# Kernel optimization log

Measured on AMD Instinct MI355X. Metric: run time of the kernel, lower is better.

## Reference

```python
import jax, jax.numpy as jnp
import numpy as np

D_MODEL = 1024
NUM_HEADS = 16
D_K = D_MODEL // NUM_HEADS


def setup_inputs() -> dict:
    key = jax.random.key(0)
    ks = jax.random.split(key, 9)
    s = 1.0 / np.sqrt(D_MODEL)
    x = jax.random.normal(ks[0], (2, 2048, D_MODEL), dtype=jnp.float32)
    Wq = jax.random.uniform(ks[1], (D_MODEL, D_MODEL), jnp.float32, -s, s)
    bq = jax.random.uniform(ks[2], (D_MODEL,), jnp.float32, -s, s)
    Wk = jax.random.uniform(ks[3], (D_MODEL, D_MODEL), jnp.float32, -s, s)
    bk = jax.random.uniform(ks[4], (D_MODEL,), jnp.float32, -s, s)
    Wv = jax.random.uniform(ks[5], (D_MODEL, D_MODEL), jnp.float32, -s, s)
    bv = jax.random.uniform(ks[6], (D_MODEL,), jnp.float32, -s, s)
    Wo = jax.random.uniform(ks[7], (D_MODEL, D_MODEL), jnp.float32, -s, s)
    bo = jax.random.uniform(ks[8], (D_MODEL,), jnp.float32, -s, s)
    return {"x": x, "Wq": Wq, "bq": bq, "Wk": Wk, "bk": bk,
            "Wv": Wv, "bv": bv, "Wo": Wo, "bo": bo}


def reference(x, Wq, bq, Wk, bk, Wv, bv, Wo, bo):
    B, S, _ = x.shape
    # projections (torch Linear: x @ W.T + b; here W stored as [in, out])
    q = (x @ Wq + bq).reshape(B, S, NUM_HEADS, D_K).transpose(0, 2, 1, 3)
    k = (x @ Wk + bk).reshape(B, S, NUM_HEADS, D_K).transpose(0, 2, 1, 3)
    v = (x @ Wv + bv).reshape(B, S, NUM_HEADS, D_K).transpose(0, 2, 1, 3)
    scores = jnp.einsum('bhqd,bhkd->bhqk', q, k) / jnp.sqrt(jnp.float32(D_K))
    attn = jax.nn.softmax(scores, axis=-1)
    out = jnp.einsum('bhqk,bhkd->bhqd', attn, v)  # [B,H,S,Dk]
    out = out.transpose(0, 2, 1, 3).reshape(B, S, D_MODEL)
    return out @ Wo + bo
```

## Files before the change

kernel.cpp:

```cpp
#include <hip/hip_runtime.h>
#include <hip/hip_bf16.h>

#define SEQ   2048
#define DM    1024
#define NH    16
#define DK    64
#define BATCH 2
#define M_TOT 4096
#define C1 0.18033688011112042f

typedef __attribute__((ext_vector_type(8))) short bf16x8;
typedef __attribute__((ext_vector_type(4))) float f32x4;
typedef __attribute__((ext_vector_type(16))) float f32x16;
typedef __attribute__((ext_vector_type(2))) int i32x2;
typedef unsigned short u16;

__device__ inline u16 f2b(float f) {
    union { float f; unsigned u; } x; x.f = f;
    return (u16)((x.u + 0x7FFFu + ((x.u >> 16) & 1u)) >> 16);
}

__device__ inline unsigned pk2(float a, float b) {
    __hip_bfloat162 h = __float22bfloat162_rn(make_float2(a, b));
    return *reinterpret_cast<unsigned*>(&h);
}

__device__ inline void async_cp16(const u16* g, u16* l) {
    __builtin_amdgcn_global_load_lds(
        (const __attribute__((address_space(1))) unsigned int*)g,
        (__attribute__((address_space(3))) unsigned int*)l, 16, 0, 0);
}

__device__ inline f32x16 zero16() {
    f32x16 z;
    #pragma unroll
    for (int i = 0; i < 16; ++i) z[i] = 0.f;
    return z;
}

__device__ inline bf16x8 mk8(unsigned a, unsigned b, unsigned c, unsigned d) {
    union { unsigned u[4]; bf16x8 v; } x;
    x.u[0] = a; x.u[1] = b; x.u[2] = c; x.u[3] = d;
    return x.v;
}

#define MFMA32(a, b, c) __builtin_amdgcn_mfma_f32_32x32x16_bf16(a, b, c, 0, 0, 0)

__global__ __launch_bounds__(256) void cast_x(
    const float4* __restrict__ x, uint2* __restrict__ xb)
{
    int gid = blockIdx.x * 256 + threadIdx.x;
    float4 v = x[gid];
    uint2 o;
    o.x = pk2(v.x, v.y); o.y = pk2(v.z, v.w);
    xb[gid] = o;
}

__global__ __launch_bounds__(256) void transpose_cast4(
    const float* __restrict__ W0, const float* __restrict__ W1,
    const float* __restrict__ W2, const float* __restrict__ W3,
    u16* __restrict__ WtBase)
{
    __shared__ float tile[32][33];
    const int t = threadIdx.x;
    const int n0 = blockIdx.x << 5, k0 = blockIdx.y << 5, z = blockIdx.z;
    const float* W = (z == 0) ? W0 : (z == 1) ? W1 : (z == 2) ? W2 : W3;
    u16* Wt = WtBase + (size_t)z * DM * DM;
    #pragma unroll
    for (int i = 0; i < 4; ++i) {
        int idx = t + (i << 8); int r = idx >> 5, c = idx & 31;
        tile[r][c] = W[(size_t)(k0 + r) * DM + n0 + c];
    }
    __syncthreads();
    #pragma unroll
    for (int i = 0; i < 4; ++i) {
        int idx = t + (i << 8); int r = idx >> 5, c = idx & 31;
        Wt[(size_t)(n0 + r) * DM + k0 + c] = f2b(tile[c][r]);
    }
}

__global__ __launch_bounds__(256) void gemm_bt(
    const u16* __restrict__ A, const u16* __restrict__ Bt, int mode,
    const float* __restrict__ bias0, const float* __restrict__ bias1,
    const float* __restrict__ bias2,
    void* __restrict__ out0, void* __restrict__ out1, void* __restrict__ out2)
{
    __shared__ u16 sh[16896];
    u16* As = sh;
    u16* Bs = sh + 8192;
    const int t = threadIdx.x, wid = t >> 6, lane = t & 63;
    const int lr = lane & 15, quad = lane >> 4;
    const int m0 = blockIdx.y << 7, n0 = blockIdx.x << 7;
    const int wm = (wid & 1) << 6, wn = (wid >> 1) << 6;
    const int rowA = lane >> 2;
    const int colA = (((lane & 3) - ((lane >> 3) & 3)) & 3) << 3;
    const int sA = (((lr >> 1) + quad) & 3) << 3;

    f32x4 acc[4][4];
    #pragma unroll
    for (int i = 0; i < 4; ++i)
        #pragma unroll
        for (int j = 0; j < 4; ++j) acc[i][j] = (f32x4){0.f, 0.f, 0.f, 0.f};

    auto stage = [&](int k0s, int buf) {
        #pragma unroll
        for (int i = 0; i < 2; ++i) {
            int ch = wid * 2 + i;
            async_cp16(A  + (size_t)(m0 + ch * 16 + rowA) * DM + k0s + colA,
                       As + buf * 4096 + ch * 16 * 32);
            async_cp16(Bt + (size_t)(n0 + ch * 16 + rowA) * DM + k0s + colA,
                       Bs + buf * 4096 + ch * 16 * 32);
        }
    };

    stage(0, 0);
    __syncthreads();

    for (int k0 = 0; k0 < DM; k0 += 32) {
        const int cur = (k0 >> 5) & 1;
        if (k0 + 32 < DM) stage(k0 + 32, cur ^ 1);

        const u16* Ac = As + cur * 4096;
        const u16* Bc = Bs + cur * 4096;
        bf16x8 af[4], bfr[4];
        #pragma unroll
        for (int mt = 0; mt < 4; ++mt)
            af[mt] = *(const bf16x8*)(Ac + (wm + 16 * mt + lr) * 32 + sA);
        #pragma unroll
        for (int nt = 0; nt < 4; ++nt)
            bfr[nt] = *(const bf16x8*)(Bc + (wn + 16 * nt + lr) * 32 + sA);
        #pragma unroll
        for (int mt = 0; mt < 4; ++mt)
            #pragma unroll
            for (int nt = 0; nt < 4; ++nt)
                acc[mt][nt] = __builtin_amdgcn_mfma_f32_16x16x32_bf16(
                    af[mt], bfr[nt], acc[mt][nt], 0, 0, 0);
        __syncthreads();
    }

    if (mode == 1) {
        u16* wstrip = sh + wid * 1152;
        const int ngb = n0 + wn;
        const int which = ngb >> 10, nnb = ngb & 1023;
        const int h = nnb >> 6;
        const float* bp = (which == 0) ? bias0 : (which == 1) ? bias1 : bias2;
        const float sc = (which == 0) ? C1 : 1.0f;
        float bias_v[4];
        #pragma unroll
        for (int nt = 0; nt < 4; ++nt) bias_v[nt] = bp[nnb + 16 * nt + lr];

        if (which != 1) {
            u16* dst = (which == 0) ? (u16*)out0 : (u16*)out2;
            #pragma unroll
            for (int mt = 0; mt < 4; ++mt) {
                #pragma unroll
                for (int nt = 0; nt < 4; ++nt) {
                    uint2 w;
                    w.x = pk2((acc[mt][nt][0] + bias_v[nt]) * sc,
                              (acc[mt][nt][1] + bias_v[nt]) * sc);
                    w.y = pk2((acc[mt][nt][2] + bias_v[nt]) * sc,
                              (acc[mt][nt][3] + bias_v[nt]) * sc);
                    *(uint2*)(wstrip + (16 * nt + lr) * 16 + quad * 4) = w;
                }
                asm volatile("s_waitcnt lgkmcnt(0)" ::: "memory");
                #pragma unroll
                for (int half = 0; half < 2; ++half) {
                    int id = lane + 64 * half;
                    int d = id >> 1, cho = (id & 1) << 3;
                    int m = m0 + wm + 16 * mt + cho;
                    int b = m >> 11, s = m & (SEQ - 1);
                    *(uint4*)(dst + ((size_t)(b * NH + h) * DK + d) * SEQ + s) =
                        *(const uint4*)(wstrip + d * 16 + cho);
                }
                asm volatile("s_waitcnt lgkmcnt(0)" ::: "memory");
            }
        } else {
            u16* dst = (u16*)out1;
            #pragma unroll
            for (int mt = 0; mt < 4; ++mt) {
                #pragma unroll
                for (int nt = 0; nt < 4; ++nt)
                    #pragma unroll
                    for (int r = 0; r < 4; ++r)
                        wstrip[(quad * 4 + r) * 72 + 16 * nt + lr] =
                            f2b(acc[mt][nt][r] + bias_v[nt]);
                asm volatile("s_waitcnt lgkmcnt(0)" ::: "memory");
                #pragma unroll
                for (int half = 0; half < 2; ++half) {
                    int id = lane + 64 * half;
                    int mloc = id >> 3, dl = (id & 7) << 3;
                    int m = m0 + wm + 16 * mt + mloc;
                    int b = m >> 11, s = m & (SEQ - 1);
                    *(uint4*)(dst + ((size_t)(b * NH + h) * SEQ + s) * DK + dl) =
                        *(const uint4*)(wstrip + mloc * 72 + dl);
                }
                asm volatile("s_waitcnt lgkmcnt(0)" ::: "memory");
            }
        }
    } else {
        float* O = (float*)out0;
        float* strip = (float*)sh + wid * 1088;
        float bias_v[4];
        #pragma unroll
        for (int nt = 0; nt < 4; ++nt) bias_v[nt] = bias0[n0 + wn + 16 * nt + lr];
        #pragma unroll
        for (int mt = 0; mt < 4; ++mt) {
            #pragma unroll
            for (int nt = 0; nt < 4; ++nt)
                #pragma unroll
                for (int r = 0; r < 4; ++r)
                    strip[(quad * 4 + r) * 68 + 16 * nt + lr] =
                        acc[mt][nt][r] + bias_v[nt];
            asm volatile("s_waitcnt lgkmcnt(0)" ::: "memory");
            #pragma unroll
            for (int rr = 0; rr < 4; ++rr) {
                int row = lane >> 2, chunk = (lane & 3) + 4 * rr;
                float4 v = *(const float4*)(strip + row * 68 + chunk * 4);
                *(float4*)(O + (size_t)(m0 + wm + 16 * mt + row) * DM
                             + n0 + wn + chunk * 4) = v;
            }
            asm volatile("s_waitcnt lgkmcnt(0)" ::: "memory");
        }
    }
}

__global__ __launch_bounds__(512) void attn_mfma(
    const u16* __restrict__ Qt, const u16* __restrict__ K,
    const u16* __restrict__ Vt, u16* __restrict__ A)
{
    __shared__ u16 sh[33280];

    const int t = threadIdx.x, wid = t >> 6, lane = t & 63;
    const int l31 = lane & 31, hi = lane >> 5, l7 = lane & 7;
    const int g = wid >> 2, wq = wid & 3;
    const int bx = blockIdx.x;
    const int xcd = bx & 7, within = bx >> 3;
    const int bh  = xcd * 4 + (within >> 4);
    const int q0  = (within & 15) << 7;

    const u16* Kb = K  + (size_t)bh * SEQ * DK;
    const u16* Vb = Vt + (size_t)bh * DK * SEQ;

    const int qw = q0 + 32 * wq + l31;
    const u16* Qb = Qt + (size_t)bh * DK * SEQ + qw;
    bf16x8 bQ[4];
    #pragma unroll
    for (int s = 0; s < 4; ++s)
        #pragma unroll
        for (int j = 0; j < 8; ++j)
            bQ[s][j] = (short)Qb[(size_t)(16 * s + 8 * hi + j) * SEQ];

    f32x16 O0 = zero16(), O1 = zero16();
    float lr = 0.f;

    const int w8row = wid * 8 + (lane >> 3);
    const int scol  = ((l7 ^ (lane >> 3)) << 3);

    const int rA = l31 * 64;
    int cks[4];
    #pragma unroll
    for (int s = 0; s < 4; ++s) cks[s] = ((2 * s + hi) ^ l7) << 3;

    auto stage = [&](int sit, int buf) {
        const int kt = sit << 7;
        u16* kd = sh + (buf << 13) + wid * 512;
        u16* vd = sh + 16384 + (buf << 13) + wid * 512;
        async_cp16(Kb + (size_t)(kt + w8row) * DK + scol,       kd);
        async_cp16(Kb + (size_t)(kt + 64 + w8row) * DK + scol,  kd + 4096);
        async_cp16(Vb + (size_t)w8row * SEQ + kt + scol,        vd);
        async_cp16(Vb + (size_t)w8row * SEQ + kt + 64 + scol,   vd + 4096);
    };

    stage(0, 0);
    __syncthreads();

    for (int sit = 0; sit < SEQ / 128; ++sit) {
        const u16* kbp = sh + ((sit & 1) << 13) + (g << 12) + rA;
        const u16* vbp = sh + 16384 + ((sit & 1) << 13) + (g << 12) + rA;
        if (sit + 1 < SEQ / 128) stage(sit + 1, (sit + 1) & 1);

        f32x16 Sv[2];
        __builtin_amdgcn_s_setprio(1);
        {
            bf16x8 a;
            Sv[0] = zero16();
            a = *(const bf16x8*)(kbp + cks[0]); Sv[0] = MFMA32(a, bQ[0], Sv[0]);
            a = *(const bf16x8*)(kbp + cks[1]); Sv[0] = MFMA32(a, bQ[1], Sv[0]);
            a = *(const bf16x8*)(kbp + cks[2]); Sv[0] = MFMA32(a, bQ[2], Sv[0]);
            a = *(const bf16x8*)(kbp + cks[3]); Sv[0] = MFMA32(a, bQ[3], Sv[0]);
            Sv[1] = zero16();
            a = *(const bf16x8*)(kbp + 2048 + cks[0]); Sv[1] = MFMA32(a, bQ[0], Sv[1]);
            a = *(const bf16x8*)(kbp + 2048 + cks[1]); Sv[1] = MFMA32(a, bQ[1], Sv[1]);
            a = *(const bf16x8*)(kbp + 2048 + cks[2]); Sv[1] = MFMA32(a, bQ[2], Sv[1]);
            a = *(const bf16x8*)(kbp + 2048 + cks[3]); Sv[1] = MFMA32(a, bQ[3], Sv[1]);
        }
        __builtin_amdgcn_s_setprio(0);

        unsigned pa[4][4];
        #pragma unroll
        for (int kvt = 0; kvt < 2; ++kvt) {
            float e[16];
            #pragma unroll
            for (int r = 0; r < 16; ++r)
                e[r] = __builtin_amdgcn_exp2f(Sv[kvt][r]);
            lr += (((e[0] + e[1]) + (e[2] + e[3])) +
                   ((e[4] + e[5]) + (e[6] + e[7]))) +
                  (((e[8] + e[9]) + (e[10] + e[11])) +
                   ((e[12] + e[13]) + (e[14] + e[15])));
            unsigned pk8[8];
            #pragma unroll
            for (int i = 0; i < 8; ++i) pk8[i] = pk2(e[2 * i], e[2 * i + 1]);
            #pragma unroll
            for (int ww = 0; ww < 2; ++ww) {
                i32x2 r0 = __builtin_amdgcn_permlane32_swap(
                    (int)pk8[4 * ww + 0], (int)pk8[4 * ww + 2], false, false);
                i32x2 r1 = __builtin_amdgcn_permlane32_swap(
                    (int)pk8[4 * ww + 1], (int)pk8[4 * ww + 3], false, false);
                const int w = 2 * kvt + ww;
                pa[w][0] = (unsigned)r0[0]; pa[w][1] = (unsigned)r1[0];
                pa[w][2] = (unsigned)r0[1]; pa[w][3] = (unsigned)r1[1];
            }
        }

        __builtin_amdgcn_s_setprio(1);
        #pragma unroll
        for (int w = 0; w < 4; ++w) {
            bf16x8 pw = mk8(pa[w][0], pa[w][1], pa[w][2], pa[w][3]);
            bf16x8 v0 = *(const bf16x8*)(vbp + cks[w]);
            bf16x8 v1 = *(const bf16x8*)(vbp + 2048 + cks[w]);
            O0 = MFMA32(pw, v0, O0);
            O1 = MFMA32(pw, v1, O1);
        }
        __builtin_amdgcn_s_setprio(0);

        __syncthreads();
    }

    lr += __shfl_xor(lr, 32);

    float* lred = (float*)(sh + 32768);
    if (g == 1) {
        float* red = (float*)sh + wq * 2048;
        #pragma unroll
        for (int c = 0; c < 4; ++c) {
            float4 v0 = make_float4(O0[4*c], O0[4*c+1], O0[4*c+2], O0[4*c+3]);
            float4 v1 = make_float4(O1[4*c], O1[4*c+1], O1[4*c+2], O1[4*c+3]);
            *(float4*)(red + lane * 32 + ((c ^ l7) << 2))       = v0;
            *(float4*)(red + lane * 32 + (((c + 4) ^ l7) << 2)) = v1;
        }
        if (hi == 0) lred[wq * 32 + l31] = lr;
    }
    __syncthreads();

    if (g == 0) {
        float* red = (float*)sh + wq * 2048;
        #pragma unroll
        for (int c = 0; c < 4; ++c) {
            float4 v0 = *(const float4*)(red + lane * 32 + ((c ^ l7) << 2));
            float4 v1 = *(const float4*)(red + lane * 32 + (((c + 4) ^ l7) << 2));
            O0[4*c] += v0.x; O0[4*c+1] += v0.y; O0[4*c+2] += v0.z; O0[4*c+3] += v0.w;
            O1[4*c] += v1.x; O1[4*c+1] += v1.y; O1[4*c+2] += v1.z; O1[4*c+3] += v1.w;
        }
        lr += lred[wq * 32 + l31];

        float* lt = (float*)(sh + 33024) + wq * 32;
        lt[l31] = lr;
        asm volatile("s_waitcnt lgkmcnt(0)" ::: "memory");

        const int b = bh >> 4, h = bh & 15;
        u16* Ab = A + (size_t)b * SEQ * DM + h * DK + l31;
        #pragma unroll
        for (int r = 0; r < 16; ++r) {
            const int qr = (r & 3) + 8 * (r >> 2) + 4 * hi;
            const float inv = 1.f / lt[qr];
            u16* dst = Ab + (size_t)(q0 + 32 * wq + qr) * DM;
            dst[0]  = f2b(O0[r] * inv);
            dst[32] = f2b(O1[r] * inv);
        }
    }
}

extern "C" void kernel_launch(void* const* d_in, const int* in_sizes, int n_in,
                              void* d_out, int out_size, void* d_ws, size_t ws_size,
                              hipStream_t stream)
{
    const float* x  = (const float*)d_in[0];
    const float* Wq = (const float*)d_in[1];
    const float* bq = (const float*)d_in[2];
    const float* Wk = (const float*)d_in[3];
    const float* bk = (const float*)d_in[4];
    const float* Wv = (const float*)d_in[5];
    const float* bv = (const float*)d_in[6];
    const float* Wo = (const float*)d_in[7];
    const float* bo = (const float*)d_in[8];

    const size_t NE = (size_t)M_TOT * DM;
    u16* xb     = (u16*)d_ws;
    u16* wt_qkv = xb + NE;
    u16* wt_o   = wt_qkv + 3 * (size_t)DM * DM;
    u16* qt_ws  = wt_o + (size_t)DM * DM;
    u16* k_ws   = qt_ws + NE;
    u16* vt_ws  = k_ws + NE;
    u16* a_ws   = vt_ws + NE;

    cast_x<<<M_TOT * DM / 4 / 256, 256, 0, stream>>>((const float4*)x, (uint2*)xb);
    transpose_cast4<<<dim3(32, 32, 4), 256, 0, stream>>>(Wq, Wk, Wv, Wo, wt_qkv);

    gemm_bt<<<dim3(24, 32), 256, 0, stream>>>(
        xb, wt_qkv, 1, bq, bk, bv, qt_ws, k_ws, vt_ws);

    attn_mfma<<<dim3(512), 512, 0, stream>>>(qt_ws, k_ws, vt_ws, a_ws);

    gemm_bt<<<dim3(8, 32), 256, 0, stream>>>(
        a_ws, wt_o, 0, bo, nullptr, nullptr, d_out, nullptr, nullptr);
}
```

Baseline: 191.2 us.

## Fuse prep kernels, add dedicated output GEMM, shrink attention LDS for occupancy

Merges the x cast and weight transpose into one prep launch, removing a kernel launch. Adds a dedicated output-projection GEMM with 64x128 tiles so the 4096x1024 output gets more blocks than the old 128x128 path. In attention, V is now single-buffered while K stays double-buffered, and a launch-bounds occupancy hint is added. The smaller LDS footprint is meant to fit more blocks per CU, at the cost of an extra barrier per iteration and less overlap of the V load.

```diff
diff --git a/kernel.cpp b/kernel.cpp
--- a/kernel.cpp
+++ b/kernel.cpp
@@ -46,24 +46,24 @@
 
 #define MFMA32(a, b, c) __builtin_amdgcn_mfma_f32_32x32x16_bf16(a, b, c, 0, 0, 0)
 
-__global__ __launch_bounds__(256) void cast_x(
-    const float4* __restrict__ x, uint2* __restrict__ xb)
-{
-    int gid = blockIdx.x * 256 + threadIdx.x;
-    float4 v = x[gid];
-    uint2 o;
-    o.x = pk2(v.x, v.y); o.y = pk2(v.z, v.w);
-    xb[gid] = o;
-}
-
-__global__ __launch_bounds__(256) void transpose_cast4(
+__global__ __launch_bounds__(256) void prep(
+    const float* __restrict__ x, uint2* __restrict__ xb,
     const float* __restrict__ W0, const float* __restrict__ W1,
     const float* __restrict__ W2, const float* __restrict__ W3,
     u16* __restrict__ WtBase)
 {
     __shared__ float tile[32][33];
-    const int t = threadIdx.x;
-    const int n0 = blockIdx.x << 5, k0 = blockIdx.y << 5, z = blockIdx.z;
+    const int t = threadIdx.x, z = blockIdx.z;
+    if (z >= 4) {
+        int bid = ((z - 4) << 10) + (blockIdx.y << 5) + blockIdx.x;
+        int gid = bid * 256 + t;
+        float4 v = ((const float4*)x)[gid];
+        uint2 o;
+        o.x = pk2(v.x, v.y); o.y = pk2(v.z, v.w);
+        xb[gid] = o;
+        return;
+    }
+    const int n0 = blockIdx.x << 5, k0 = blockIdx.y << 5;
     const float* W = (z == 0) ? W0 : (z == 1) ? W1 : (z == 2) ? W2 : W3;
     u16* Wt = WtBase + (size_t)z * DM * DM;
     #pragma unroll
@@ -138,7 +138,7 @@
         __syncthreads();
     }
 
-    if (mode == 1) {
+    {
         u16* wstrip = sh + wid * 1152;
         const int ngb = n0 + wn;
         const int which = ngb >> 10, nnb = ngb & 1023;
@@ -197,38 +197,94 @@
                 asm volatile("s_waitcnt lgkmcnt(0)" ::: "memory");
             }
         }
-    } else {
-        float* O = (float*)out0;
-        float* strip = (float*)sh + wid * 1088;
-        float bias_v[4];
-        #pragma unroll
-        for (int nt = 0; nt < 4; ++nt) bias_v[nt] = bias0[n0 + wn + 16 * nt + lr];
-        #pragma unroll
-        for (int mt = 0; mt < 4; ++mt) {
-            #pragma unroll
-            for (int nt = 0; nt < 4; ++nt)
-                #pragma unroll
-                for (int r = 0; r < 4; ++r)
-                    strip[(quad * 4 + r) * 68 + 16 * nt + lr] =
-                        acc[mt][nt][r] + bias_v[nt];
-            asm volatile("s_waitcnt lgkmcnt(0)" ::: "memory");
-            #pragma unroll
-            for (int rr = 0; rr < 4; ++rr) {
-                int row = lane >> 2, chunk = (lane & 3) + 4 * rr;
-                float4 v = *(const float4*)(strip + row * 68 + chunk * 4);
-                *(float4*)(O + (size_t)(m0 + wm + 16 * mt + row) * DM
-                             + n0 + wn + chunk * 4) = v;
-            }
-            asm volatile("s_waitcnt lgkmcnt(0)" ::: "memory");
-        }
-    }
-}
-
-__global__ __launch_bounds__(512) void attn_mfma(
+    }
+}
+
+__global__ __launch_bounds__(256) void gemm_o(
+    const u16* __restrict__ A, const u16* __restrict__ Bt,
+    const float* __restrict__ bias, float* __restrict__ O)
+{
+    __shared__ u16 sh[12288];
+    u16* As = sh;
+    u16* Bs = sh + 4096;
+    const int t = threadIdx.x, wid = t >> 6, lane = t & 63;
+    const int lr = lane & 15, quad = lane >> 4;
+    const int m0 = blockIdx.y << 6, n0 = blockIdx.x << 7;
+    const int wn = wid << 5;
+    const int rowA = lane >> 2;
+    const int colA = (((lane & 3) - ((lane >> 3) & 3)) & 3) << 3;
+    const int sA = (((lr >> 1) + quad) & 3) << 3;
+
+    f32x4 acc[4][2];
+    #pragma unroll
+    for (int i = 0; i < 4; ++i)
+        #pragma unroll
+        for (int j = 0; j < 2; ++j) acc[i][j] = (f32x4){0.f, 0.f, 0.f, 0.f};
+
+    auto stage = [&](int k0s, int buf) {
+        async_cp16(A + (size_t)(m0 + wid * 16 + rowA) * DM + k0s + colA,
+                   As + buf * 2048 + wid * 512);
+        async_cp16(Bt + (size_t)(n0 + (2 * wid) * 16 + rowA) * DM + k0s + colA,
+                   Bs + buf * 4096 + (2 * wid) * 512);
+        async_cp16(Bt + (size_t)(n0 + (2 * wid + 1) * 16 + rowA) * DM + k0s + colA,
+                   Bs + buf * 4096 + (2 * wid + 1) * 512);
+    };
+
+    stage(0, 0);
+    __syncthreads();
+
+    for (int k0 = 0; k0 < DM; k0 += 32) {
+        const int cur = (k0 >> 5) & 1;
+        if (k0 + 32 < DM) stage(k0 + 32, cur ^ 1);
+
+        const u16* Ac = As + cur * 2048;
+        const u16* Bc = Bs + cur * 4096;
+        bf16x8 af[4], bfr[2];
+        #pragma unroll
+        for (int mt = 0; mt < 4; ++mt)
+            af[mt] = *(const bf16x8*)(Ac + (16 * mt + lr) * 32 + sA);
+        #pragma unroll
+        for (int nt = 0; nt < 2; ++nt)
+            bfr[nt] = *(const bf16x8*)(Bc + (wn + 16 * nt + lr) * 32 + sA);
+        #pragma unroll
+        for (int mt = 0; mt < 4; ++mt)
+            #pragma unroll
+            for (int nt = 0; nt < 2; ++nt)
+                acc[mt][nt] = __builtin_amdgcn_mfma_f32_16x16x32_bf16(
+                    af[mt], bfr[nt], acc[mt][nt], 0, 0, 0);
+        __syncthreads();
+    }
+
+    float bias_v[2];
+    #pragma unroll
+    for (int nt = 0; nt < 2; ++nt) bias_v[nt] = bias[n0 + wn + 16 * nt + lr];
+    float* strip = (float*)sh + wid * 576;
+    #pragma unroll
+    for (int mt = 0; mt < 4; ++mt) {
+        #pragma unroll
+        for (int nt = 0; nt < 2; ++nt)
+            #pragma unroll
+            for (int r = 0; r < 4; ++r)
+                strip[(quad * 4 + r) * 36 + 16 * nt + lr] =
+                    acc[mt][nt][r] + bias_v[nt];
+        asm volatile("s_waitcnt lgkmcnt(0)" ::: "memory");
+        #pragma unroll
+        for (int rr = 0; rr < 2; ++rr) {
+            int id = lane + 64 * rr;
+            int row = id >> 3, ch = id & 7;
+            float4 v = *(const float4*)(strip + row * 36 + ch * 4);
+            *(float4*)(O + (size_t)(m0 + 16 * mt + row) * DM
+                         + n0 + wn + ch * 4) = v;
+        }
+        asm volatile("s_waitcnt lgkmcnt(0)" ::: "memory");
+    }
+}
+
+__global__ __launch_bounds__(512, 6) void attn_mfma(
     const u16* __restrict__ Qt, const u16* __restrict__ K,
     const u16* __restrict__ Vt, u16* __restrict__ A)
 {
-    __shared__ u16 sh[33280];
+    __shared__ u16 sh[25088];
 
     const int t = threadIdx.x, wid = t >> 6, lane = t & 63;
     const int l31 = lane & 31, hi = lane >> 5, l7 = lane & 7;
@@ -251,6 +307,7 @@
             bQ[s][j] = (short)Qb[(size_t)(16 * s + 8 * hi + j) * SEQ];
 
     f32x16 O0 = zero16(), O1 = zero16();
+    const f32x16 Z = zero16();
     float lr = 0.f;
 
     const int w8row = wid * 8 + (lane >> 3);
@@ -261,35 +318,35 @@
     #pragma unroll
     for (int s = 0; s < 4; ++s) cks[s] = ((2 * s + hi) ^ l7) << 3;
 
-    auto stage = [&](int sit, int buf) {
+    auto stageK = [&](int sit, int buf) {
         const int kt = sit << 7;
         u16* kd = sh + (buf << 13) + wid * 512;
-        u16* vd = sh + 16384 + (buf << 13) + wid * 512;
-        async_cp16(Kb + (size_t)(kt + w8row) * DK + scol,       kd);
-        async_cp16(Kb + (size_t)(kt + 64 + w8row) * DK + scol,  kd + 4096);
-        async_cp16(Vb + (size_t)w8row * SEQ + kt + scol,        vd);
-        async_cp16(Vb + (size_t)w8row * SEQ + kt + 64 + scol,   vd + 4096);
+        async_cp16(Kb + (size_t)(kt + w8row) * DK + scol,      kd);
+        async_cp16(Kb + (size_t)(kt + 64 + w8row) * DK + scol, kd + 4096);
     };
-
-    stage(0, 0);
+    auto stageV = [&](int sit) {
+        const int kt = sit << 7;
+        u16* vd = sh + 16384 + wid * 512;
+        async_cp16(Vb + (size_t)w8row * SEQ + kt + scol,      vd);
+        async_cp16(Vb + (size_t)w8row * SEQ + kt + 64 + scol, vd + 4096);
+    };
+
+    stageK(0, 0); stageK(1, 1); stageV(0);
     __syncthreads();
 
     for (int sit = 0; sit < SEQ / 128; ++sit) {
         const u16* kbp = sh + ((sit & 1) << 13) + (g << 12) + rA;
-        const u16* vbp = sh + 16384 + ((sit & 1) << 13) + (g << 12) + rA;
-        if (sit + 1 < SEQ / 128) stage(sit + 1, (sit + 1) & 1);
+        const u16* vbp = sh + 16384 + (g << 12) + rA;
 
         f32x16 Sv[2];
         __builtin_amdgcn_s_setprio(1);
         {
             bf16x8 a;
-            Sv[0] = zero16();
-            a = *(const bf16x8*)(kbp + cks[0]); Sv[0] = MFMA32(a, bQ[0], Sv[0]);
-            a = *(const bf16x8*)(kbp + cks[1]); Sv[0] = MFMA32(a, bQ[1], Sv[0]);
-            a = *(const bf16x8*)(kbp + cks[2]); Sv[0] = MFMA32(a, bQ[2], Sv[0]);
-            a = *(const bf16x8*)(kbp + cks[3]); Sv[0] = MFMA32(a, bQ[3], Sv[0]);
-            Sv[1] = zero16();
-            a = *(const bf16x8*)(kbp + 2048 + cks[0]); Sv[1] = MFMA32(a, bQ[0], Sv[1]);
+            a = *(const bf16x8*)(kbp + cks[0]);        Sv[0] = MFMA32(a, bQ[0], Z);
+            a = *(const bf16x8*)(kbp + cks[1]);        Sv[0] = MFMA32(a, bQ[1], Sv[0]);
+            a = *(const bf16x8*)(kbp + cks[2]);        Sv[0] = MFMA32(a, bQ[2], Sv[0]);
+            a = *(const bf16x8*)(kbp + cks[3]);        Sv[0] = MFMA32(a, bQ[3], Sv[0]);
+            a = *(const bf16x8*)(kbp + 2048 + cks[0]); Sv[1] = MFMA32(a, bQ[0], Z);
             a = *(const bf16x8*)(kbp + 2048 + cks[1]); Sv[1] = MFMA32(a, bQ[1], Sv[1]);
             a = *(const bf16x8*)(kbp + 2048 + cks[2]); Sv[1] = MFMA32(a, bQ[2], Sv[1]);
             a = *(const bf16x8*)(kbp + 2048 + cks[3]); Sv[1] = MFMA32(a, bQ[3], Sv[1]);
@@ -322,6 +379,8 @@
             }
         }
 
+        __syncthreads();
+
         __builtin_amdgcn_s_setprio(1);
         #pragma unroll
         for (int w = 0; w < 4; ++w) {
@@ -334,11 +393,15 @@
         __builtin_amdgcn_s_setprio(0);
 
         __syncthreads();
+
+        if (sit + 2 < SEQ / 128) stageK(sit + 2, sit & 1);
+        if (sit + 1 < SEQ / 128) stageV(sit + 1);
     }
 
     lr += __shfl_xor(lr, 32);
 
-    float* lred = (float*)(sh + 32768);
+    float* lred = (float*)(sh + 24576);
+    float* lt   = (float*)(sh + 24832);
     if (g == 1) {
         float* red = (float*)sh + wq * 2048;
         #pragma unroll
@@ -363,8 +426,7 @@
         }
         lr += lred[wq * 32 + l31];
 
-        float* lt = (float*)(sh + 33024) + wq * 32;
-        lt[l31] = lr;
+        lt[wq * 32 + l31] = lr;
         asm volatile("s_waitcnt lgkmcnt(0)" ::: "memory");
 
         const int b = bh >> 4, h = bh & 15;
@@ -372,7 +434,7 @@
         #pragma unroll
         for (int r = 0; r < 16; ++r) {
             const int qr = (r & 3) + 8 * (r >> 2) + 4 * hi;
-            const float inv = 1.f / lt[qr];
+            const float inv = 1.f / lt[wq * 32 + qr];
             u16* dst = Ab + (size_t)(q0 + 32 * wq + qr) * DM;
             dst[0]  = f2b(O0[r] * inv);
             dst[32] = f2b(O1[r] * inv);
@@ -403,14 +465,13 @@
     u16* vt_ws  = k_ws + NE;
     u16* a_ws   = vt_ws + NE;
 
-    cast_x<<<M_TOT * DM / 4 / 256, 256, 0, stream>>>((const float4*)x, (uint2*)xb);
-    transpose_cast4<<<dim3(32, 32, 4), 256, 0, stream>>>(Wq, Wk, Wv, Wo, wt_qkv);
+    prep<<<dim3(32, 32, 8), 256, 0, stream>>>(
+        x, (uint2*)xb, Wq, Wk, Wv, Wo, wt_qkv);
 
     gemm_bt<<<dim3(24, 32), 256, 0, stream>>>(
         xb, wt_qkv, 1, bq, bk, bv, qt_ws, k_ws, vt_ws);
 
     attn_mfma<<<dim3(512), 512, 0, stream>>>(qt_ws, k_ws, vt_ws, a_ws);
 
-    gemm_bt<<<dim3(8, 32), 256, 0, stream>>>(
-        a_ws, wt_o, 0, bo, nullptr, nullptr, d_out, nullptr, nullptr);
-}
+    gemm_o<<<dim3(8, 64), 256, 0, stream>>>(a_ws, wt_o, bo, (float*)d_out);
+}
```

After: 324.4 us. +69.6%, slower.
